# Kernel tuning notes

Hardware: AMD Instinct MI355X
Metric: run time of the kernel (lower is better)

The kernel has to match this reference:

```python
import jax, jax.numpy as jnp
import numpy as np

B, N, C, M = 2, 16384, 256, 16  # M = win_w*win_h for stage 1
W = N // M

def setup_inputs() -> dict:
    key = jax.random.key(0)
    ks = jax.random.split(key, 8)
    s = 1.0 / np.sqrt(C)
    return {
        "input": jax.random.normal(ks[0], (B, N, C), jnp.float32),
        "embed_qk": jax.random.normal(ks[1], (B, W, M, M, 3), jnp.float32),
        "Wq": jax.random.normal(ks[2], (C, C), jnp.float32) * s,
        "bq": jax.random.normal(ks[3], (C,), jnp.float32) * 0.01,
        "Wk": jax.random.normal(ks[4], (C, C), jnp.float32) * s,
        "bk": jax.random.normal(ks[5], (C,), jnp.float32) * 0.01,
        "Wp": jax.random.normal(ks[6], (3, 1), jnp.float32) * 0.5,
        "bp": jax.random.normal(ks[7], (1,), jnp.float32) * 0.01,
    }

def reference(input, embed_qk, Wq, bq, Wk, bk, Wp, bp):
    WIN = 16  # stage==1 -> win_w*win_h = 4*4
    b, n, c = input.shape
    add = (-n) % WIN
    q = jax.nn.elu(input @ Wq + bq) + 1.0
    k = jax.nn.elu(input @ Wk + bk) + 1.0
    v = input
    pad = ((0, 0), (0, add), (0, 0))
    q_win = jnp.pad(q, pad).reshape(b, -1, WIN, c)
    k_win = jnp.pad(k, pad).reshape(b, -1, WIN, c)
    v_win = jnp.pad(v, pad).reshape(b, -1, WIN, c)
    # second ELU+1 feature map (as in the original)
    phi_q = jax.nn.elu(q_win) + 1.0
    phi_k = jax.nn.elu(k_win) + 1.0
    # KV sums over ALL windows w -> (b, m, c, d)
    KV = jnp.einsum('bwmc,bwmd->bmcd', phi_k, v_win)
    # (b, w, n, m, d) expanded intermediate
    att = jnp.einsum('bwnc,bmcd->bwnmd', phi_q, KV)
    p = (embed_qk @ Wp + bp)[..., 0]  # (b, w, m, m)
    att = att + p[..., None]
    out = att.reshape(b, -1, c)[:, :n, :]
    return out
```

## Files before the change

### kernel.cpp

```cpp
#include <hip/hip_runtime.h>

typedef __attribute__((ext_vector_type(8))) short s16x8;
typedef __attribute__((ext_vector_type(8))) ushort u16x8;
typedef __attribute__((ext_vector_type(4))) ushort u16x4;
typedef __attribute__((ext_vector_type(4))) float f32x4v;

namespace {

constexpr int kB = 2;
constexpr int kN = 16384;
constexpr int kC = 256;
constexpr int kQR = 1024;

__device__ __forceinline__ ushort f2bf(float f) {
  union { float f; uint u; } v; v.f = f;
  uint u = v.u + 0x7fffu + ((v.u >> 16) & 1u);
  return (ushort)(u >> 16);
}

__device__ __forceinline__ float phi_act(float x) {
  return x > 0.f ? x + 2.f : __expf(x) + 1.f;
}

__global__ __launch_bounds__(256) void wt_kernel(const float* __restrict__ Wq,
                                                 const float* __restrict__ Wk,
                                                 ushort* __restrict__ WqT,
                                                 ushort* __restrict__ WkT) {
  __shared__ float ts[64][65];
  const float* W = blockIdx.z ? Wk : Wq;
  ushort* WT = blockIdx.z ? WkT : WqT;
  const int bi = blockIdx.x, bj = blockIdx.y, t = threadIdx.x;
  for (int rep = 0; rep < 16; ++rep) {
    int e = rep * 256 + t, r = e >> 6, c = e & 63;
    ts[r][c] = W[(size_t)(bi * 64 + r) * kC + bj * 64 + c];
  }
  __syncthreads();
  for (int rep = 0; rep < 16; ++rep) {
    int e = rep * 256 + t, j = e >> 6, k = e & 63;
    WT[(size_t)(bj * 64 + j) * kC + bi * 64 + k] = f2bf(ts[k][j]);
  }
}

__global__ __launch_bounds__(512) void proj_fused(
    const float* __restrict__ X, const ushort* __restrict__ WqT,
    const ushort* __restrict__ WkT, const float* __restrict__ bq,
    const float* __restrict__ bk, ushort* __restrict__ xg,
    ushort* __restrict__ kg, ushort* __restrict__ qf) {
  __shared__ __align__(16) ushort smem[24576];

  const int t = threadIdx.x, lane = t & 63, wv = t >> 6;
  const int bx = blockIdx.x;
  const bool kmode = bx < 256;
  int b, n0;
  const ushort* WT;
  const float* bias;
  if (kmode) {
    b = bx >> 7; n0 = (bx & 127) * 128; WT = WkT; bias = bk;
  } else {
    int i = bx - 256; b = i >> 3; n0 = (i & 7) * 128; WT = WqT; bias = bq;
  }
  const int wgrp = bx & 127;
  const float* Xbase = X + ((size_t)b * kN + n0) * kC;

  const int m = t >> 5, cl = t & 31;
  const int bj = t >> 2, bch = t & 3;

  float fa[8];
  u16x8 rb0, rb1;
  auto stageLoad = [&](int ks) {
    const int k0 = ks * 32;
#pragma unroll
    for (int wl = 0; wl < 8; ++wl)
      fa[wl] = Xbase[(size_t)(wl * 16 + m) * kC + k0 + cl];
    rb0 = *reinterpret_cast<const u16x8*>(WT + (size_t)bj * kC + k0 + bch * 8);
    rb1 = *reinterpret_cast<const u16x8*>(WT + (size_t)(bj + 128) * kC + k0 + bch * 8);
  };
  auto stageWrite = [&](int h, int ks) {
    ushort* A = smem + h * 4096;
    ushort* B = smem + 8192 + h * 8192;
    u16x8 vx;
#pragma unroll
    for (int wl = 0; wl < 8; ++wl) {
      int row = wl * 16 + m;
      ushort bf = f2bf(fa[wl]);
      A[row * 32 + (((cl >> 3) ^ ((row >> 1) & 3)) << 3) + (cl & 7)] = bf;
      vx[wl] = bf;
    }
    *reinterpret_cast<u16x8*>(B + bj * 32 + ((bch ^ ((bj >> 1) & 3)) << 3)) = rb0;
    *reinterpret_cast<u16x8*>(B + (bj + 128) * 32 + ((bch ^ (((bj + 128) >> 1) & 3)) << 3)) = rb1;
    if (kmode) {
      *reinterpret_cast<u16x8*>(
          xg + (((size_t)(b * 16 + m) * 128 + wgrp) * 256 + ks * 32 + cl) * 8) = vx;
    }
  };

  f32x4v acc[4][4] = {};
  const int lo = lane & 15, hi = lane >> 4;
  const int wr0 = (wv >> 2) * 64, wc0 = (wv & 3) * 64;
  auto mma = [&](int h) {
    const ushort* A = smem + h * 4096;
    const ushort* B = smem + 8192 + h * 8192;
    s16x8 af[4], bf[4];
#pragma unroll
    for (int i = 0; i < 4; ++i) {
      int r = wr0 + i * 16 + lo;
      af[i] = *reinterpret_cast<const s16x8*>(A + r * 32 + ((hi ^ ((r >> 1) & 3)) << 3));
    }
#pragma unroll
    for (int j = 0; j < 4; ++j) {
      int cj = wc0 + j * 16 + lo;
      bf[j] = *reinterpret_cast<const s16x8*>(B + cj * 32 + ((hi ^ ((cj >> 1) & 3)) << 3));
    }
#pragma unroll
    for (int i = 0; i < 4; ++i)
#pragma unroll
      for (int j = 0; j < 4; ++j)
        acc[i][j] = __builtin_amdgcn_mfma_f32_16x16x32_bf16(af[i], bf[j], acc[i][j], 0, 0, 0);
  };

  stageLoad(0);
  stageWrite(0, 0);
  __syncthreads();
  int cur = 0;
  for (int ks = 0; ks < 8; ++ks) {
    if (ks < 7) stageLoad(ks + 1);
    __builtin_amdgcn_sched_barrier(0);
    mma(cur);
    __builtin_amdgcn_sched_barrier(0);
    if (ks < 7) stageWrite(cur ^ 1, ks + 1);
    __syncthreads();
    cur ^= 1;
  }

  float bv[4];
#pragma unroll
  for (int fj = 0; fj < 4; ++fj) bv[fj] = bias[wc0 + fj * 16 + lo];

  if (kmode) {
    u16x8 vout[8];
    ushort* ep = smem;
#pragma unroll
    for (int h = 0; h < 2; ++h) {
      __syncthreads();
      if ((wv >> 2) == h) {
#pragma unroll
        for (int fi = 0; fi < 4; ++fi)
#pragma unroll
          for (int fj = 0; fj < 4; ++fj)
#pragma unroll
            for (int r4 = 0; r4 < 4; ++r4) {
              int rl = fi * 16 + hi * 4 + r4;
              int col = wc0 + fj * 16 + lo;
              ep[rl * 260 + col] = f2bf(phi_act(acc[fi][fj][r4] + bv[fj]));
            }
      }
      __syncthreads();
#pragma unroll
      for (int j = 0; j < 8; ++j) {
        int c = j * 32 + cl;
#pragma unroll
        for (int wl = 0; wl < 4; ++wl)
          vout[j][h * 4 + wl] = ep[(wl * 16 + m) * 260 + c];
      }
    }
#pragma unroll
    for (int j = 0; j < 8; ++j) {
      int c = j * 32 + cl;
      *reinterpret_cast<u16x8*>(
          kg + (((size_t)(b * 16 + m) * 128 + wgrp) * 256 + c) * 8) = vout[j];
    }
  } else {
#pragma unroll
    for (int fi = 0; fi < 4; ++fi)
#pragma unroll
      for (int fj = 0; fj < 4; ++fj)
#pragma unroll
        for (int r4 = 0; r4 < 4; ++r4) {
          int row = n0 + wr0 + fi * 16 + hi * 4 + r4;
          int col = wc0 + fj * 16 + lo;
          qf[((size_t)b * kQR + row) * kC + col] = f2bf(phi_act(acc[fi][fj][r4] + bv[fj]));
        }
  }
}

__global__ __launch_bounds__(256) void kv_kernel(const ushort* __restrict__ kg,
                                                 const ushort* __restrict__ xg,
                                                 ushort* __restrict__ kvt) {
  __shared__ __align__(16) ushort smem[16384];
  const int t = threadIdx.x, lane = t & 63, wv = t >> 6;
  const int cb = blockIdx.x, db = blockIdx.y, bm = blockIdx.z;
  const int lc = t & 63, g2 = t >> 6;

  u16x8 ra0, ra1, rb0, rb1;
  auto stageLoad = [&](int ws) {
    size_t base = (size_t)bm * 128 + ws * 8;
    ra0 = *reinterpret_cast<const u16x8*>(kg + ((base + g2) * 256 + cb * 64 + lc) * 8);
    ra1 = *reinterpret_cast<const u16x8*>(kg + ((base + g2 + 4) * 256 + cb * 64 + lc) * 8);
    rb0 = *reinterpret_cast<const u16x8*>(xg + ((base + g2) * 256 + db * 64 + lc) * 8);
    rb1 = *reinterpret_cast<const u16x8*>(xg + ((base + g2 + 4) * 256 + db * 64 + lc) * 8);
  };
  auto stageWrite = [&](int h) {
    ushort* A = smem + h * 4096;
    ushort* B = smem + 8192 + h * 4096;
    int s = (lc >> 1) & 7;
    *reinterpret_cast<u16x8*>(A + lc * 64 + ((g2 ^ s) << 3)) = ra0;
    *reinterpret_cast<u16x8*>(A + lc * 64 + (((g2 + 4) ^ s) << 3)) = ra1;
    *reinterpret_cast<u16x8*>(B + lc * 64 + ((g2 ^ s) << 3)) = rb0;
    *reinterpret_cast<u16x8*>(B + lc * 64 + (((g2 + 4) ^ s) << 3)) = rb1;
  };

  f32x4v acc[2][2] = {};
  const int lo = lane & 15, hi = lane >> 4;
  const int wr0 = (wv >> 1) * 32, wc0 = (wv & 1) * 32;
  auto mma = [&](int h) {
    const ushort* A = smem + h * 4096;
    const ushort* B = smem + 8192 + h * 4096;
    s16x8 af[2][2], bf[2][2];
#pragma unroll
    for (int i = 0; i < 2; ++i) {
      int r = wr0 + i * 16 + lo;
      int s = (r >> 1) & 7;
#pragma unroll
      for (int kk = 0; kk < 2; ++kk)
        af[i][kk] = *reinterpret_cast<const s16x8*>(A + r * 64 + (((kk * 4 + hi) ^ s) << 3));
    }
#pragma unroll
    for (int j = 0; j < 2; ++j) {
      int c = wc0 + j * 16 + lo;
      int s = (c >> 1) & 7;
#pragma unroll
      for (int kk = 0; kk < 2; ++kk)
        bf[j][kk] = *reinterpret_cast<const s16x8*>(B + c * 64 + (((kk * 4 + hi) ^ s) << 3));
    }
#pragma unroll
    for (int kk = 0; kk < 2; ++kk)
#pragma unroll
      for (int i = 0; i < 2; ++i)
#pragma unroll
        for (int j = 0; j < 2; ++j)
          acc[i][j] = __builtin_amdgcn_mfma_f32_16x16x32_bf16(af[i][kk], bf[j][kk], acc[i][j], 0, 0, 0);
  };

  stageLoad(0);
  stageWrite(0);
  __syncthreads();
  int cur = 0;
  for (int ws = 0; ws < 16; ++ws) {
    if (ws < 15) stageLoad(ws + 1);
    __builtin_amdgcn_sched_barrier(0);
    mma(cur);
    __builtin_amdgcn_sched_barrier(0);
    if (ws < 15) stageWrite(cur ^ 1);
    __syncthreads();
    cur ^= 1;
  }
#pragma unroll
  for (int i = 0; i < 2; ++i)
#pragma unroll
    for (int j = 0; j < 2; ++j) {
      int d = db * 64 + wc0 + j * 16 + lo;
      int c = cb * 64 + wr0 + i * 16 + hi * 4;
      u16x4 v = {f2bf(acc[i][j][0]), f2bf(acc[i][j][1]), f2bf(acc[i][j][2]),
                 f2bf(acc[i][j][3])};
      *reinterpret_cast<u16x4*>(kvt + ((size_t)bm * 256 + d) * 256 + c) = v;
    }
}

__global__ __launch_bounds__(256) void out_kernel(
    const ushort* __restrict__ qf, const ushort* __restrict__ kvt,
    const float* __restrict__ EQK, const float* __restrict__ Wp,
    const float* __restrict__ bp, float* __restrict__ Out) {
  __shared__ __align__(16) ushort smem[16384];
  __shared__ float Ps[128];
  const int t = threadIdx.x, lane = t & 63, wv = t >> 6;
  const int qb = blockIdx.x, db = blockIdx.y, bm = blockIdx.z;
  const int b = bm >> 4, mm = bm & 15;
  if (t < 128) {
    int qr = qb * 128 + t;
    const float* e = EQK + (((size_t)(b * 1024 + (qr >> 4)) * 16 + (qr & 15)) * 16 + mm) * 3;
    Ps[t] = e[0] * Wp[0] + e[1] * Wp[1] + e[2] * Wp[2] + bp[0];
  }
  const int r2 = t >> 2, ch = t & 3;

  u16x8 ra0, ra1, rb0, rb1;
  auto stageLoad = [&](int ks) {
    int k0 = ks * 32;
    const ushort* Aq = qf + ((size_t)b * kQR + qb * 128) * kC;
    const ushort* Bk = kvt + ((size_t)bm * 256 + db * 128) * kC;
    ra0 = *reinterpret_cast<const u16x8*>(Aq + (size_t)r2 * kC + k0 + ch * 8);
    ra1 = *reinterpret_cast<const u16x8*>(Aq + (size_t)(r2 + 64) * kC + k0 + ch * 8);
    rb0 = *reinterpret_cast<const u16x8*>(Bk + (size_t)r2 * kC + k0 + ch * 8);
    rb1 = *reinterpret_cast<const u16x8*>(Bk + (size_t)(r2 + 64) * kC + k0 + ch * 8);
  };
  auto stageWrite = [&](int h) {
    ushort* A = smem + h * 4096;
    ushort* B = smem + 8192 + h * 4096;
    *reinterpret_cast<u16x8*>(A + r2 * 32 + ((ch ^ ((r2 >> 1) & 3)) << 3)) = ra0;
    *reinterpret_cast<u16x8*>(A + (r2 + 64) * 32 + ((ch ^ (((r2 + 64) >> 1) & 3)) << 3)) = ra1;
    *reinterpret_cast<u16x8*>(B + r2 * 32 + ((ch ^ ((r2 >> 1) & 3)) << 3)) = rb0;
    *reinterpret_cast<u16x8*>(B + (r2 + 64) * 32 + ((ch ^ (((r2 + 64) >> 1) & 3)) << 3)) = rb1;
  };

  f32x4v acc[4][4] = {};
  const int lo = lane & 15, hi = lane >> 4;
  const int wr0 = (wv >> 1) * 64, wc0 = (wv & 1) * 64;
  auto mma = [&](int h) {
    const ushort* A = smem + h * 4096;
    const ushort* B = smem + 8192 + h * 4096;
    s16x8 af[4], bf[4];
#pragma unroll
    for (int i = 0; i < 4; ++i) {
      int r = wr0 + i * 16 + lo;
      af[i] = *reinterpret_cast<const s16x8*>(A + r * 32 + ((hi ^ ((r >> 1) & 3)) << 3));
    }
#pragma unroll
    for (int j = 0; j < 4; ++j) {
      int c = wc0 + j * 16 + lo;
      bf[j] = *reinterpret_cast<const s16x8*>(B + c * 32 + ((hi ^ ((c >> 1) & 3)) << 3));
    }
#pragma unroll
    for (int i = 0; i < 4; ++i)
#pragma unroll
      for (int j = 0; j < 4; ++j)
        acc[i][j] = __builtin_amdgcn_mfma_f32_16x16x32_bf16(af[i], bf[j], acc[i][j], 0, 0, 0);
  };

  stageLoad(0);
  stageWrite(0);
  __syncthreads();
  int cur = 0;
  for (int ks = 0; ks < 8; ++ks) {
    if (ks < 7) stageLoad(ks + 1);
    __builtin_amdgcn_sched_barrier(0);
    mma(cur);
    __builtin_amdgcn_sched_barrier(0);
    if (ks < 7) stageWrite(cur ^ 1);
    __syncthreads();
    cur ^= 1;
  }
#pragma unroll
  for (int fi = 0; fi < 4; ++fi)
#pragma unroll
    for (int r4 = 0; r4 < 4; ++r4) {
      int rowl = wr0 + fi * 16 + hi * 4 + r4;
      int qr = qb * 128 + rowl;
      float p = Ps[rowl];
      size_t orow = ((size_t)b * kN + (size_t)qr * 16 + mm) * kC;
#pragma unroll
      for (int fj = 0; fj < 4; ++fj) {
        int d = db * 128 + wc0 + fj * 16 + lo;
        Out[orow + d] = acc[fi][fj][r4] + p;
      }
    }
}

}

extern "C" void kernel_launch(void* const* d_in, const int* in_sizes, int n_in,
                              void* d_out, int out_size, void* d_ws,
                              size_t ws_size, hipStream_t stream) {
  const float* input = (const float*)d_in[0];
  const float* eqk = (const float*)d_in[1];
  const float* Wq = (const float*)d_in[2];
  const float* bq = (const float*)d_in[3];
  const float* Wk = (const float*)d_in[4];
  const float* bk = (const float*)d_in[5];
  const float* Wp = (const float*)d_in[6];
  const float* bp = (const float*)d_in[7];
  float* out = (float*)d_out;

  ushort* ws = (ushort*)d_ws;
  ushort* WqT = ws;
  ushort* WkT = WqT + 65536;
  ushort* xg = WkT + 65536;
  ushort* kg = xg + 8388608;
  ushort* qf = kg + 8388608;
  ushort* kvt = qf + 524288;

  wt_kernel<<<dim3(4, 4, 2), 256, 0, stream>>>(Wq, Wk, WqT, WkT);
  proj_fused<<<dim3(272), 512, 0, stream>>>(input, WqT, WkT, bq, bk, xg, kg, qf);
  kv_kernel<<<dim3(4, 4, 32), 256, 0, stream>>>(kg, xg, kvt);
  out_kernel<<<dim3(8, 2, 32), 256, 0, stream>>>(qf, kvt, eqk, Wp, bp, out);
}
```

Before: 143.7 us.

## Split V regrouping into separate kernel, vectorize projection loads, swizzle block order

The bf16 window-grouped copy of the input is now produced by a dedicated regroup kernel that stages through LDS. The projection kernel can therefore load X with coalesced float4 reads and write to LDS with 16-byte vectors, instead of strided scalar loads plus a side store. kv_kernel and out_kernel switch to 1D grids with a swizzled block-to-tile mapping so that blocks sharing data are spread across XCDs. The cost is an extra launch and a second full read of X.

New measurement: 145.9 us. About the same (+1.5%).

```diff
diff --git a/kernel.cpp b/kernel.cpp
--- a/kernel.cpp
+++ b/kernel.cpp
@@ -41,11 +41,42 @@
   }
 }
 
+__global__ __launch_bounds__(256) void regroup_kernel(const float* __restrict__ X,
+                                                      ushort* __restrict__ G) {
+  __shared__ ushort ls[64 * 288];
+  const int cb = blockIdx.x;
+  const int wb = blockIdx.y;
+  const int b = blockIdx.z;
+  const int t = threadIdx.x;
+  const float* src = X + ((size_t)b * kN + wb * 1024) * kC + cb * 16;
+  const int lr = t >> 2, cg = t & 3;
+  for (int rep = 0; rep < 16; ++rep) {
+    int row = rep * 64 + lr;
+    float4 v = *reinterpret_cast<const float4*>(src + (size_t)row * kC + cg * 4);
+    int w = row >> 4, m = row & 15;
+    int base = w * 288 + m * 18 + cg * 4;
+    uint p0 = (uint)f2bf(v.x) | ((uint)f2bf(v.y) << 16);
+    uint p1 = (uint)f2bf(v.z) | ((uint)f2bf(v.w) << 16);
+    *reinterpret_cast<uint*>(ls + base) = p0;
+    *reinterpret_cast<uint*>(ls + base + 2) = p1;
+  }
+  __syncthreads();
+  const int m = t >> 4, c_l = t & 15;
+  const size_t gbase = ((size_t)b * 16 + m) * 128 + wb * 8;
+#pragma unroll
+  for (int r = 0; r < 8; ++r) {
+    u16x8 v;
+#pragma unroll
+    for (int wl = 0; wl < 8; ++wl) v[wl] = ls[(r * 8 + wl) * 288 + m * 18 + c_l];
+    *reinterpret_cast<u16x8*>(G + (gbase + r) * 2048 + (size_t)(cb * 16 + c_l) * 8) = v;
+  }
+}
+
 __global__ __launch_bounds__(512) void proj_fused(
     const float* __restrict__ X, const ushort* __restrict__ WqT,
     const ushort* __restrict__ WkT, const float* __restrict__ bq,
-    const float* __restrict__ bk, ushort* __restrict__ xg,
-    ushort* __restrict__ kg, ushort* __restrict__ qf) {
+    const float* __restrict__ bk, ushort* __restrict__ kg,
+    ushort* __restrict__ qf) {
   __shared__ __align__(16) ushort smem[24576];
 
   const int t = threadIdx.x, lane = t & 63, wv = t >> 6;
@@ -62,36 +93,27 @@
   const int wgrp = bx & 127;
   const float* Xbase = X + ((size_t)b * kN + n0) * kC;
 
-  const int m = t >> 5, cl = t & 31;
+  const int r4 = t >> 2, ca = (t & 3) << 3;
   const int bj = t >> 2, bch = t & 3;
 
-  float fa[8];
+  float4 fa0, fa1;
   u16x8 rb0, rb1;
   auto stageLoad = [&](int ks) {
     const int k0 = ks * 32;
-#pragma unroll
-    for (int wl = 0; wl < 8; ++wl)
-      fa[wl] = Xbase[(size_t)(wl * 16 + m) * kC + k0 + cl];
+    fa0 = *reinterpret_cast<const float4*>(Xbase + (size_t)r4 * kC + k0 + ca);
+    fa1 = *reinterpret_cast<const float4*>(Xbase + (size_t)r4 * kC + k0 + ca + 4);
     rb0 = *reinterpret_cast<const u16x8*>(WT + (size_t)bj * kC + k0 + bch * 8);
     rb1 = *reinterpret_cast<const u16x8*>(WT + (size_t)(bj + 128) * kC + k0 + bch * 8);
   };
-  auto stageWrite = [&](int h, int ks) {
+  auto stageWrite = [&](int h) {
     ushort* A = smem + h * 4096;
     ushort* B = smem + 8192 + h * 8192;
-    u16x8 vx;
-#pragma unroll
-    for (int wl = 0; wl < 8; ++wl) {
-      int row = wl * 16 + m;
-      ushort bf = f2bf(fa[wl]);
-      A[row * 32 + (((cl >> 3) ^ ((row >> 1) & 3)) << 3) + (cl & 7)] = bf;
-      vx[wl] = bf;
-    }
+    u16x8 va;
+    va[0] = f2bf(fa0.x); va[1] = f2bf(fa0.y); va[2] = f2bf(fa0.z); va[3] = f2bf(fa0.w);
+    va[4] = f2bf(fa1.x); va[5] = f2bf(fa1.y); va[6] = f2bf(fa1.z); va[7] = f2bf(fa1.w);
+    *reinterpret_cast<u16x8*>(A + r4 * 32 + (((t & 3) ^ ((r4 >> 1) & 3)) << 3)) = va;
     *reinterpret_cast<u16x8*>(B + bj * 32 + ((bch ^ ((bj >> 1) & 3)) << 3)) = rb0;
     *reinterpret_cast<u16x8*>(B + (bj + 128) * 32 + ((bch ^ (((bj + 128) >> 1) & 3)) << 3)) = rb1;
-    if (kmode) {
-      *reinterpret_cast<u16x8*>(
-          xg + (((size_t)(b * 16 + m) * 128 + wgrp) * 256 + ks * 32 + cl) * 8) = vx;
-    }
   };
 
   f32x4v acc[4][4] = {};
@@ -119,7 +141,7 @@
   };
 
   stageLoad(0);
-  stageWrite(0, 0);
+  stageWrite(0);
   __syncthreads();
   int cur = 0;
   for (int ks = 0; ks < 8; ++ks) {
@@ -127,7 +149,7 @@
     __builtin_amdgcn_sched_barrier(0);
     mma(cur);
     __builtin_amdgcn_sched_barrier(0);
-    if (ks < 7) stageWrite(cur ^ 1, ks + 1);
+    if (ks < 7) stageWrite(cur ^ 1);
     __syncthreads();
     cur ^= 1;
   }
@@ -137,6 +159,7 @@
   for (int fj = 0; fj < 4; ++fj) bv[fj] = bias[wc0 + fj * 16 + lo];
 
   if (kmode) {
+    const int m = t >> 5, cl = t & 31;
     u16x8 vout[8];
     ushort* ep = smem;
 #pragma unroll
@@ -148,10 +171,10 @@
 #pragma unroll
           for (int fj = 0; fj < 4; ++fj)
 #pragma unroll
-            for (int r4 = 0; r4 < 4; ++r4) {
-              int rl = fi * 16 + hi * 4 + r4;
+            for (int r = 0; r < 4; ++r) {
+              int rl = fi * 16 + hi * 4 + r;
               int col = wc0 + fj * 16 + lo;
-              ep[rl * 260 + col] = f2bf(phi_act(acc[fi][fj][r4] + bv[fj]));
+              ep[rl * 260 + col] = f2bf(phi_act(acc[fi][fj][r] + bv[fj]));
             }
       }
       __syncthreads();
@@ -175,10 +198,10 @@
 #pragma unroll
       for (int fj = 0; fj < 4; ++fj)
 #pragma unroll
-        for (int r4 = 0; r4 < 4; ++r4) {
-          int row = n0 + wr0 + fi * 16 + hi * 4 + r4;
+        for (int r = 0; r < 4; ++r) {
+          int row = n0 + wr0 + fi * 16 + hi * 4 + r;
           int col = wc0 + fj * 16 + lo;
-          qf[((size_t)b * kQR + row) * kC + col] = f2bf(phi_act(acc[fi][fj][r4] + bv[fj]));
+          qf[((size_t)b * kQR + row) * kC + col] = f2bf(phi_act(acc[fi][fj][r] + bv[fj]));
         }
   }
 }
@@ -188,7 +211,8 @@
                                                  ushort* __restrict__ kvt) {
   __shared__ __align__(16) ushort smem[16384];
   const int t = threadIdx.x, lane = t & 63, wv = t >> 6;
-  const int cb = blockIdx.x, db = blockIdx.y, bm = blockIdx.z;
+  const int swz = (blockIdx.x & 7) * 64 + (blockIdx.x >> 3);
+  const int bm = swz >> 4, cb = swz & 3, db = (swz >> 2) & 3;
   const int lc = t & 63, g2 = t >> 6;
 
   u16x8 ra0, ra1, rb0, rb1;
@@ -273,7 +297,8 @@
   __shared__ __align__(16) ushort smem[16384];
   __shared__ float Ps[128];
   const int t = threadIdx.x, lane = t & 63, wv = t >> 6;
-  const int qb = blockIdx.x, db = blockIdx.y, bm = blockIdx.z;
+  const int swz = (blockIdx.x & 7) * 64 + (blockIdx.x >> 3);
+  const int bm = swz >> 4, qb = swz & 7, db = (swz >> 3) & 1;
   const int b = bm >> 4, mm = bm & 15;
   if (t < 128) {
     int qr = qb * 128 + t;
@@ -378,7 +403,8 @@
   ushort* kvt = qf + 524288;
 
   wt_kernel<<<dim3(4, 4, 2), 256, 0, stream>>>(Wq, Wk, WqT, WkT);
-  proj_fused<<<dim3(272), 512, 0, stream>>>(input, WqT, WkT, bq, bk, xg, kg, qf);
-  kv_kernel<<<dim3(4, 4, 32), 256, 0, stream>>>(kg, xg, kvt);
-  out_kernel<<<dim3(8, 2, 32), 256, 0, stream>>>(qf, kvt, eqk, Wp, bp, out);
-}
+  regroup_kernel<<<dim3(16, 16, 2), 256, 0, stream>>>(input, xg);
+  proj_fused<<<dim3(272), 512, 0, stream>>>(input, WqT, WkT, bq, bk, kg, qf);
+  kv_kernel<<<dim3(512), 256, 0, stream>>>(kg, xg, kvt);
+  out_kernel<<<dim3(512), 256, 0, stream>>>(qf, kvt, eqk, Wp, bp, out);
+}
```

## Use direct global-to-LDS loads in kv_kernel and swizzle block mapping for XCD locality

Applied to the files above, without the earlier changes.

kv_kernel now loads K and X tiles straight into LDS with global_load_lds, skipping the register round trip. It uses a larger double buffer holding 16 window rows per stage, which halves the number of stages. Both kv_kernel and out_kernel switch to a 1D grid with a block-index swizzle, so blocks sharing the same bm land on the same XCD and can reuse its L2. LDS use doubles, which may lower occupancy, and the LDS layout drops the XOR swizzle, which risks bank conflicts.

New measurement: 133.5 us. 7.1% less time.

```diff
diff --git a/kernel.cpp b/kernel.cpp
--- a/kernel.cpp
+++ b/kernel.cpp
@@ -20,6 +20,12 @@
 
 __device__ __forceinline__ float phi_act(float x) {
   return x > 0.f ? x + 2.f : __expf(x) + 1.f;
+}
+
+__device__ __forceinline__ void gl16(const ushort* g, ushort* l) {
+  __builtin_amdgcn_global_load_lds(
+      (const __attribute__((address_space(1))) void*)g,
+      (__attribute__((address_space(3))) void*)l, 16, 0, 0);
 }
 
 __global__ __launch_bounds__(256) void wt_kernel(const float* __restrict__ Wq,
@@ -186,82 +192,65 @@
 __global__ __launch_bounds__(256) void kv_kernel(const ushort* __restrict__ kg,
                                                  const ushort* __restrict__ xg,
                                                  ushort* __restrict__ kvt) {
-  __shared__ __align__(16) ushort smem[16384];
+  __shared__ __align__(16) ushort smem[32768];
   const int t = threadIdx.x, lane = t & 63, wv = t >> 6;
-  const int cb = blockIdx.x, db = blockIdx.y, bm = blockIdx.z;
-  const int lc = t & 63, g2 = t >> 6;
-
-  u16x8 ra0, ra1, rb0, rb1;
-  auto stageLoad = [&](int ws) {
-    size_t base = (size_t)bm * 128 + ws * 8;
-    ra0 = *reinterpret_cast<const u16x8*>(kg + ((base + g2) * 256 + cb * 64 + lc) * 8);
-    ra1 = *reinterpret_cast<const u16x8*>(kg + ((base + g2 + 4) * 256 + cb * 64 + lc) * 8);
-    rb0 = *reinterpret_cast<const u16x8*>(xg + ((base + g2) * 256 + db * 64 + lc) * 8);
-    rb1 = *reinterpret_cast<const u16x8*>(xg + ((base + g2 + 4) * 256 + db * 64 + lc) * 8);
-  };
-  auto stageWrite = [&](int h) {
-    ushort* A = smem + h * 4096;
-    ushort* B = smem + 8192 + h * 4096;
-    int s = (lc >> 1) & 7;
-    *reinterpret_cast<u16x8*>(A + lc * 64 + ((g2 ^ s) << 3)) = ra0;
-    *reinterpret_cast<u16x8*>(A + lc * 64 + (((g2 + 4) ^ s) << 3)) = ra1;
-    *reinterpret_cast<u16x8*>(B + lc * 64 + ((g2 ^ s) << 3)) = rb0;
-    *reinterpret_cast<u16x8*>(B + lc * 64 + (((g2 + 4) ^ s) << 3)) = rb1;
-  };
-
-  f32x4v acc[2][2] = {};
+  const int swz = (blockIdx.x & 7) * 64 + (blockIdx.x >> 3);
+  const int bm = swz >> 4, cb = swz & 3, db = (swz >> 2) & 3;
+  const int c_l = t & 63;
+  const ushort* Abase = kg + (size_t)bm * 262144 + (size_t)(cb * 64) * 8;
+  const ushort* Bbase = xg + (size_t)bm * 262144 + (size_t)(db * 64) * 8;
+
+  auto STAGE = [&](int h, int s) {
+    ushort* A = smem + h * 8192;
+    ushort* B = smem + 16384 + h * 8192;
+#pragma unroll
+    for (int i = 0; i < 4; ++i) {
+      int o = i * 4 + wv;
+      size_t goff = ((size_t)(s * 16 + o) * 256 + c_l) * 8;
+      int loff = (i * 256 + t) * 8;
+      gl16(Abase + goff, A + loff);
+      gl16(Bbase + goff, B + loff);
+    }
+  };
+
   const int lo = lane & 15, hi = lane >> 4;
   const int wr0 = (wv >> 1) * 32, wc0 = (wv & 1) * 32;
-  auto mma = [&](int h) {
-    const ushort* A = smem + h * 4096;
-    const ushort* B = smem + 8192 + h * 4096;
-    s16x8 af[2][2], bf[2][2];
-#pragma unroll
-    for (int i = 0; i < 2; ++i) {
-      int r = wr0 + i * 16 + lo;
-      int s = (r >> 1) & 7;
-#pragma unroll
-      for (int kk = 0; kk < 2; ++kk)
-        af[i][kk] = *reinterpret_cast<const s16x8*>(A + r * 64 + (((kk * 4 + hi) ^ s) << 3));
-    }
-#pragma unroll
-    for (int j = 0; j < 2; ++j) {
-      int c = wc0 + j * 16 + lo;
-      int s = (c >> 1) & 7;
-#pragma unroll
-      for (int kk = 0; kk < 2; ++kk)
-        bf[j][kk] = *reinterpret_cast<const s16x8*>(B + c * 64 + (((kk * 4 + hi) ^ s) << 3));
-    }
-#pragma unroll
-    for (int kk = 0; kk < 2; ++kk)
-#pragma unroll
-      for (int i = 0; i < 2; ++i)
-#pragma unroll
-        for (int j = 0; j < 2; ++j)
-          acc[i][j] = __builtin_amdgcn_mfma_f32_16x16x32_bf16(af[i][kk], bf[j][kk], acc[i][j], 0, 0, 0);
-  };
-
-  stageLoad(0);
-  stageWrite(0);
+  f32x4v acc[2][2] = {};
+  auto MMA = [&](int h) {
+    const ushort* A = smem + h * 8192;
+    const ushort* B = smem + 16384 + h * 8192;
+#pragma unroll
+    for (int kk = 0; kk < 4; ++kk) {
+      const int o = kk * 4 + hi;
+      s16x8 a0 = *reinterpret_cast<const s16x8*>(A + o * 512 + (wr0 + lo) * 8);
+      s16x8 a1 = *reinterpret_cast<const s16x8*>(A + o * 512 + (wr0 + 16 + lo) * 8);
+      s16x8 b0 = *reinterpret_cast<const s16x8*>(B + o * 512 + (wc0 + lo) * 8);
+      s16x8 b1 = *reinterpret_cast<const s16x8*>(B + o * 512 + (wc0 + 16 + lo) * 8);
+      acc[0][0] = __builtin_amdgcn_mfma_f32_16x16x32_bf16(a0, b0, acc[0][0], 0, 0, 0);
+      acc[0][1] = __builtin_amdgcn_mfma_f32_16x16x32_bf16(a0, b1, acc[0][1], 0, 0, 0);
+      acc[1][0] = __builtin_amdgcn_mfma_f32_16x16x32_bf16(a1, b0, acc[1][0], 0, 0, 0);
+      acc[1][1] = __builtin_amdgcn_mfma_f32_16x16x32_bf16(a1, b1, acc[1][1], 0, 0, 0);
+    }
+  };
+
+  STAGE(0, 0);
   __syncthreads();
   int cur = 0;
-  for (int ws = 0; ws < 16; ++ws) {
-    if (ws < 15) stageLoad(ws + 1);
-    __builtin_amdgcn_sched_barrier(0);
-    mma(cur);
-    __builtin_amdgcn_sched_barrier(0);
-    if (ws < 15) stageWrite(cur ^ 1);
+  for (int s = 0; s < 8; ++s) {
+    if (s < 7) STAGE(cur ^ 1, s + 1);
+    __builtin_amdgcn_sched_barrier(0);
+    MMA(cur);
     __syncthreads();
     cur ^= 1;
   }
 #pragma unroll
-  for (int i = 0; i < 2; ++i)
-#pragma unroll
-    for (int j = 0; j < 2; ++j) {
-      int d = db * 64 + wc0 + j * 16 + lo;
-      int c = cb * 64 + wr0 + i * 16 + hi * 4;
-      u16x4 v = {f2bf(acc[i][j][0]), f2bf(acc[i][j][1]), f2bf(acc[i][j][2]),
-                 f2bf(acc[i][j][3])};
+  for (int fi = 0; fi < 2; ++fi)
+#pragma unroll
+    for (int fj = 0; fj < 2; ++fj) {
+      int d = db * 64 + wc0 + fj * 16 + lo;
+      int c = cb * 64 + wr0 + fi * 16 + hi * 4;
+      u16x4 v = {f2bf(acc[fi][fj][0]), f2bf(acc[fi][fj][1]),
+                 f2bf(acc[fi][fj][2]), f2bf(acc[fi][fj][3])};
       *reinterpret_cast<u16x4*>(kvt + ((size_t)bm * 256 + d) * 256 + c) = v;
     }
 }
@@ -273,7 +262,8 @@
   __shared__ __align__(16) ushort smem[16384];
   __shared__ float Ps[128];
   const int t = threadIdx.x, lane = t & 63, wv = t >> 6;
-  const int qb = blockIdx.x, db = blockIdx.y, bm = blockIdx.z;
+  const int swz = (blockIdx.x & 7) * 64 + (blockIdx.x >> 3);
+  const int bm = swz >> 4, qb = swz & 7, db = (swz >> 3) & 1;
   const int b = bm >> 4, mm = bm & 15;
   if (t < 128) {
     int qr = qb * 128 + t;
@@ -379,6 +369,6 @@
 
   wt_kernel<<<dim3(4, 4, 2), 256, 0, stream>>>(Wq, Wk, WqT, WkT);
   proj_fused<<<dim3(272), 512, 0, stream>>>(input, WqT, WkT, bq, bk, xg, kg, qf);
-  kv_kernel<<<dim3(4, 4, 32), 256, 0, stream>>>(kg, xg, kvt);
-  out_kernel<<<dim3(8, 2, 32), 256, 0, stream>>>(qf, kvt, eqk, Wp, bp, out);
-}
+  kv_kernel<<<dim3(512), 256, 0, stream>>>(kg, xg, kvt);
+  out_kernel<<<dim3(512), 256, 0, stream>>>(qf, kvt, eqk, Wp, bp, out);
+}
```
